# Kernel tuning notes

Measured on AMD Instinct MI355X. Metric: run time of the kernel, lower is better.

Reference implementation:

```python
import jax, jax.numpy as jnp
import numpy as np

SEQ, B, IN, H, OUT = 600, 4096, 6, 30, 61


def setup_inputs() -> dict:
    key = jax.random.key(0)
    ks = jax.random.split(key, 9)
    s_ih = 1.0 / np.sqrt(H)
    return {
        "X": jax.random.normal(ks[0], (SEQ, B, IN), dtype=jnp.float32),
        "W_ih": jax.random.uniform(ks[1], (4 * H, IN), jnp.float32, -s_ih, s_ih),
        "W_hh": jax.random.uniform(ks[2], (4 * H, H), jnp.float32, -s_ih, s_ih),
        "b_ih": jax.random.uniform(ks[3], (4 * H,), jnp.float32, -s_ih, s_ih),
        "b_hh": jax.random.uniform(ks[4], (4 * H,), jnp.float32, -s_ih, s_ih),
        "W1": jax.random.uniform(ks[5], (H, H), jnp.float32, -s_ih, s_ih),
        "b1": jax.random.uniform(ks[6], (H,), jnp.float32, -s_ih, s_ih),
        "W2": jax.random.uniform(ks[7], (OUT, H), jnp.float32, -s_ih, s_ih),
        "b2": jax.random.uniform(ks[8], (OUT,), jnp.float32, -s_ih, s_ih),
        "batch_size": B,
    }


def _lstm_last_h(X, W_ih, W_hh, b_ih, b_hh):
    # Precompute input projections for all timesteps: [T, B, 4H]
    xg = jnp.einsum("tbi,gi->tbg", X, W_ih) + b_ih + b_hh
    h0 = jnp.zeros((X.shape[1], W_hh.shape[1]), X.dtype)
    c0 = jnp.zeros_like(h0)

    def step(carry, xg_t):
        h, c = carry
        g = xg_t + h @ W_hh.T  # [B, 4H]
        i, f, gg, o = jnp.split(g, 4, axis=-1)  # PyTorch gate order i,f,g,o
        c = jax.nn.sigmoid(f) * c + jax.nn.sigmoid(i) * jnp.tanh(gg)
        h = jax.nn.sigmoid(o) * jnp.tanh(c)
        return (h, c), None

    (h, _), _ = jax.lax.scan(step, (h0, c0), xg)
    return h  # out[-1, :, :]


def reference(X, W_ih, W_hh, b_ih, b_hh, W1, b1, W2, b2, batch_size):
    h = _lstm_last_h(X, W_ih, W_hh, b_ih, b_hh)
    out = h @ W1.T + b1  # fc1
    # dropout(p=0.6) is identity in eval mode
    out = out @ W2.T + b2  # fc2
    return out  # [B, 61]
```

## Files before the change

kernel.cpp:

```cpp
#include <hip/hip_runtime.h>


#define SEQ   600
#define BATCH 4096
#define INP   6
#define HID   30
#define NOUT  61

typedef float f32x2 __attribute__((ext_vector_type(2)));

__device__ __forceinline__ float rcp_(float x)  { return __builtin_amdgcn_rcpf(x); }
__device__ __forceinline__ float exp2_(float x) { return __builtin_amdgcn_exp2f(x); }
#define LOG2E  1.4426950408889634f
#define LOG2E2 2.8853900817779268f

extern "C" __global__ void __launch_bounds__(64, 2)
lstm_fused4(const float* __restrict__ X,   const float* __restrict__ Wih,
            const float* __restrict__ Whh, const float* __restrict__ bih,
            const float* __restrict__ bhh, const float* __restrict__ W1,
            const float* __restrict__ b1,  const float* __restrict__ W2,
            const float* __restrict__ b2,  float* __restrict__ out)
{
    __shared__ float h_sh[2][32];
    __shared__ float o1_sh[2][32];

    const int lane = threadIdx.x;
    const int half = lane >> 5;
    const int u    = lane & 31;
    const int uu   = (u < HID) ? u : (HID - 1);
    const int b    = blockIdx.x * 2 + half;
    const bool act = (u < HID);

    h_sh[half][u] = 0.0f;

    const float* r0 = Whh + (0 * HID + uu) * HID;
    const float* r1 = Whh + (1 * HID + uu) * HID;
    const float* r2 = Whh + (2 * HID + uu) * HID;
    const float* r3 = Whh + (3 * HID + uu) * HID;

    f32x2 w0[15], w1[15], w2[15], w3[15];
    #pragma unroll
    for (int j = 0; j < 15; ++j) {
        asm volatile("global_load_dwordx2 %0, %1, off" : "=v"(w0[j]) : "v"(r0 + 2 * j));
        asm volatile("global_load_dwordx2 %0, %1, off" : "=v"(w1[j]) : "v"(r1 + 2 * j));
        asm volatile("global_load_dwordx2 %0, %1, off" : "=v"(w2[j]) : "v"(r2 + 2 * j));
        asm volatile("global_load_dwordx2 %0, %1, off" : "=v"(w3[j]) : "v"(r3 + 2 * j));
    }
    const float* s0 = Wih + (0 * HID + uu) * INP;
    const float* s1 = Wih + (1 * HID + uu) * INP;
    const float* s2 = Wih + (2 * HID + uu) * INP;
    const float* s3 = Wih + (3 * HID + uu) * INP;

    f32x2 xw0[3], xw1[3], xw2[3], xw3[3];
    #pragma unroll
    for (int j = 0; j < 3; ++j) {
        asm volatile("global_load_dwordx2 %0, %1, off" : "=v"(xw0[j]) : "v"(s0 + 2 * j));
        asm volatile("global_load_dwordx2 %0, %1, off" : "=v"(xw1[j]) : "v"(s1 + 2 * j));
        asm volatile("global_load_dwordx2 %0, %1, off" : "=v"(xw2[j]) : "v"(s2 + 2 * j));
        asm volatile("global_load_dwordx2 %0, %1, off" : "=v"(xw3[j]) : "v"(s3 + 2 * j));
    }
    asm volatile("s_waitcnt vmcnt(0)" ::: "memory");

    float bb0 = 0.f, bb1 = 0.f, bb2 = 0.f, bb3 = 0.f;
    if (act) {
        bb0 = bih[0 * HID + u] + bhh[0 * HID + u];
        bb1 = bih[1 * HID + u] + bhh[1 * HID + u];
        bb2 = bih[2 * HID + u] + bhh[2 * HID + u];
        bb3 = bih[3 * HID + u] + bhh[3 * HID + u];
    }
    asm volatile("" : "+v"(bb0), "+v"(bb1), "+v"(bb2), "+v"(bb3));

    float c = 0.f, h = 0.f;

    f32x2 xc0, xc1, xc2, xn0, xn1, xn2;
    {
        const f32x2* p = (const f32x2*)(X + (size_t)b * INP);
        xc0 = p[0]; xc1 = p[1]; xc2 = p[2];
    }
    asm volatile("s_waitcnt lgkmcnt(0)" ::: "memory");

    const float4* h4p = (const float4*)(&h_sh[half][0]);
    const f32x2*  h2p = (const f32x2*)(&h_sh[half][0]);

    for (int t = 0; t < SEQ; ++t) {
        const int tn = (t + 1 < SEQ) ? (t + 1) : (SEQ - 1);
        const f32x2* p = (const f32x2*)(X + ((size_t)tn * BATCH + b) * INP);
        xn0 = p[0]; xn1 = p[1]; xn2 = p[2];

        float4 H0 = h4p[0], H1 = h4p[1], H2 = h4p[2], H3 = h4p[3];
        float4 H4 = h4p[4], H5 = h4p[5], H6 = h4p[6];
        f32x2  Ht = h2p[14];

        f32x2 a0e = f32x2{bb0, 0.f}, a0o = (f32x2)0.f;
        f32x2 a1e = f32x2{bb1, 0.f}, a1o = (f32x2)0.f;
        f32x2 a2e = f32x2{bb2, 0.f}, a2o = (f32x2)0.f;
        f32x2 a3e = f32x2{bb3, 0.f}, a3o = (f32x2)0.f;

        #define PK4(J, HX, HY, E)  do {                                   \
            f32x2 hv = f32x2{HX, HY};                                     \
            a0##E = __builtin_elementwise_fma(w0[J], hv, a0##E);          \
            a1##E = __builtin_elementwise_fma(w1[J], hv, a1##E);          \
            a2##E = __builtin_elementwise_fma(w2[J], hv, a2##E);          \
            a3##E = __builtin_elementwise_fma(w3[J], hv, a3##E);          \
        } while (0)
        PK4(0,  H0.x, H0.y, e); PK4(1,  H0.z, H0.w, o);
        PK4(2,  H1.x, H1.y, e); PK4(3,  H1.z, H1.w, o);
        PK4(4,  H2.x, H2.y, e); PK4(5,  H2.z, H2.w, o);
        PK4(6,  H3.x, H3.y, e); PK4(7,  H3.z, H3.w, o);
        PK4(8,  H4.x, H4.y, e); PK4(9,  H4.z, H4.w, o);
        PK4(10, H5.x, H5.y, e); PK4(11, H5.z, H5.w, o);
        PK4(12, H6.x, H6.y, e); PK4(13, H6.z, H6.w, o);
        {
            a0e = __builtin_elementwise_fma(w0[14], Ht, a0e);
            a1e = __builtin_elementwise_fma(w1[14], Ht, a1e);
            a2e = __builtin_elementwise_fma(w2[14], Ht, a2e);
            a3e = __builtin_elementwise_fma(w3[14], Ht, a3e);
        }
        #undef PK4
        a0o = __builtin_elementwise_fma(xw0[0], xc0, a0o);
        a1o = __builtin_elementwise_fma(xw1[0], xc0, a1o);
        a2o = __builtin_elementwise_fma(xw2[0], xc0, a2o);
        a3o = __builtin_elementwise_fma(xw3[0], xc0, a3o);
        a0e = __builtin_elementwise_fma(xw0[1], xc1, a0e);
        a1e = __builtin_elementwise_fma(xw1[1], xc1, a1e);
        a2e = __builtin_elementwise_fma(xw2[1], xc1, a2e);
        a3e = __builtin_elementwise_fma(xw3[1], xc1, a3e);
        a0o = __builtin_elementwise_fma(xw0[2], xc2, a0o);
        a1o = __builtin_elementwise_fma(xw1[2], xc2, a1o);
        a2o = __builtin_elementwise_fma(xw2[2], xc2, a2o);
        a3o = __builtin_elementwise_fma(xw3[2], xc2, a3o);

        const f32x2 g0v = a0e + a0o, g1v = a1e + a1o;
        const f32x2 g2v = a2e + a2o, g3v = a3e + a3o;
        const float g0 = g0v.x + g0v.y;
        const float g1 = g1v.x + g1v.y;
        const float g2 = g2v.x + g2v.y;
        const float g3 = g3v.x + g3v.y;

        const float si = rcp_(1.0f + exp2_(-LOG2E * g0));
        const float sf = rcp_(1.0f + exp2_(-LOG2E * g1));
        const float tg = 1.0f - 2.0f * rcp_(exp2_(LOG2E2 * g2) + 1.0f);
        const float so = rcp_(1.0f + exp2_(-LOG2E * g3));

        c = fmaf(sf, c, si * tg);
        const float tc = 1.0f - 2.0f * rcp_(exp2_(LOG2E2 * c) + 1.0f);
        h = so * tc;

        if (act) h_sh[half][u] = h;
        asm volatile("s_waitcnt lgkmcnt(0)" ::: "memory");

        xc0 = xn0; xc1 = xn1; xc2 = xn2;
    }

    if (act) {
        float a1 = b1[u];
        const float* w1r = W1 + u * HID;
        #pragma unroll
        for (int k = 0; k < HID; ++k) a1 = fmaf(w1r[k], h_sh[half][k], a1);
        o1_sh[half][u] = a1;
    }
    asm volatile("s_waitcnt lgkmcnt(0)" ::: "memory");

    if (act) {
        for (int o = u; o < NOUT; o += HID) {
            float a2 = b2[o];
            const float* w2r = W2 + o * HID;
            #pragma unroll
            for (int k = 0; k < HID; ++k) a2 = fmaf(w2r[k], o1_sh[half][k], a2);
            out[(size_t)b * NOUT + o] = a2;
        }
    }
}

extern "C" void kernel_launch(void* const* d_in, const int* in_sizes, int n_in,
                              void* d_out, int out_size, void* d_ws, size_t ws_size,
                              hipStream_t stream) {
    const float* X   = (const float*)d_in[0];
    const float* Wih = (const float*)d_in[1];
    const float* Whh = (const float*)d_in[2];
    const float* bih = (const float*)d_in[3];
    const float* bhh = (const float*)d_in[4];
    const float* W1  = (const float*)d_in[5];
    const float* b1  = (const float*)d_in[6];
    const float* W2  = (const float*)d_in[7];
    const float* b2  = (const float*)d_in[8];
    float* out = (float*)d_out;

    dim3 grid(BATCH / 2);
    dim3 block(64);
    hipLaunchKernelGGL(lstm_fused4, grid, block, 0, stream,
                       X, Wih, Whh, bih, bhh, W1, b1, W2, b2, out);
}
```

Before: 350.2 us.

## Use packed fp16 dot2 for LSTM gate matvec with fp16 hidden state

Converts recurrent and input weights to packed fp16 once in registers and computes gate pre-activations with v_dot2 fp16 instructions that accumulate in fp32. The hidden state is stored in shared memory as fp16, so each step reads it with four 16-byte loads instead of seven float4 loads plus one f32x2 load. The input prefetch is restructured as a pointer walk with a peeled last step. This roughly halves the weight register footprint and the FMA count per step. The cost is reduced precision in the 600-step recurrence, and the saturating pkrtz conversion may accumulate error beyond tolerance.

After: 324.5 us. 1.08x faster.

```diff
diff --git a/kernel.cpp b/kernel.cpp
--- a/kernel.cpp
+++ b/kernel.cpp
@@ -7,21 +7,26 @@
 #define HID   30
 #define NOUT  61
 
+typedef __fp16 f16;
+typedef f16  f16x2 __attribute__((ext_vector_type(2)));
 typedef float f32x2 __attribute__((ext_vector_type(2)));
 
 __device__ __forceinline__ float rcp_(float x)  { return __builtin_amdgcn_rcpf(x); }
 __device__ __forceinline__ float exp2_(float x) { return __builtin_amdgcn_exp2f(x); }
+__device__ __forceinline__ f16x2 as_h2(unsigned v) {
+    union { unsigned u; f16x2 h; } c; c.u = v; return c.h;
+}
 #define LOG2E  1.4426950408889634f
 #define LOG2E2 2.8853900817779268f
 
 extern "C" __global__ void __launch_bounds__(64, 2)
-lstm_fused4(const float* __restrict__ X,   const float* __restrict__ Wih,
+lstm_fused9(const float* __restrict__ X,   const float* __restrict__ Wih,
             const float* __restrict__ Whh, const float* __restrict__ bih,
             const float* __restrict__ bhh, const float* __restrict__ W1,
             const float* __restrict__ b1,  const float* __restrict__ W2,
             const float* __restrict__ b2,  float* __restrict__ out)
 {
-    __shared__ float h_sh[2][32];
+    __shared__ __align__(16) f16 h_sh[2][32];
     __shared__ float o1_sh[2][32];
 
     const int lane = threadIdx.x;
@@ -31,35 +36,45 @@
     const int b    = blockIdx.x * 2 + half;
     const bool act = (u < HID);
 
-    h_sh[half][u] = 0.0f;
-
-    const float* r0 = Whh + (0 * HID + uu) * HID;
-    const float* r1 = Whh + (1 * HID + uu) * HID;
-    const float* r2 = Whh + (2 * HID + uu) * HID;
-    const float* r3 = Whh + (3 * HID + uu) * HID;
-
-    f32x2 w0[15], w1[15], w2[15], w3[15];
+    h_sh[half][u] = (f16)0.f;
+
+    f16x2 w0[15], w1[15], w2[15], w3[15];
+    f16x2 x0w[3], x1w[3], x2w[3], x3w[3];
+
+    #define LOADGATE(Q, WH, XW) do {                                          \
+        const float* rr = Whh + (Q * HID + uu) * HID;                         \
+        const float* ss = Wih + (Q * HID + uu) * INP;                         \
+        f32x2 t[15], tx[3];                                                   \
+        _Pragma("unroll")                                                     \
+        for (int j = 0; j < 15; ++j)                                          \
+            asm volatile("global_load_dwordx2 %0, %1, off"                    \
+                         : "=v"(t[j]) : "v"(rr + 2 * j));                     \
+        _Pragma("unroll")                                                     \
+        for (int j = 0; j < 3; ++j)                                           \
+            asm volatile("global_load_dwordx2 %0, %1, off"                    \
+                         : "=v"(tx[j]) : "v"(ss + 2 * j));                    \
+        asm volatile("s_waitcnt vmcnt(0)" ::: "memory");                      \
+        __builtin_amdgcn_sched_barrier(0);      \
+        _Pragma("unroll")                                                     \
+        for (int j = 0; j < 15; ++j)                                          \
+            WH[j] = __builtin_amdgcn_cvt_pkrtz(t[j].x, t[j].y);               \
+        _Pragma("unroll")                                                     \
+        for (int j = 0; j < 3; ++j)                                           \
+            XW[j] = __builtin_amdgcn_cvt_pkrtz(tx[j].x, tx[j].y);             \
+    } while (0)
+
+    LOADGATE(0, w0, x0w);
+    LOADGATE(1, w1, x1w);
+    LOADGATE(2, w2, x2w);
+    LOADGATE(3, w3, x3w);
+    #undef LOADGATE
+
     #pragma unroll
-    for (int j = 0; j < 15; ++j) {
-        asm volatile("global_load_dwordx2 %0, %1, off" : "=v"(w0[j]) : "v"(r0 + 2 * j));
-        asm volatile("global_load_dwordx2 %0, %1, off" : "=v"(w1[j]) : "v"(r1 + 2 * j));
-        asm volatile("global_load_dwordx2 %0, %1, off" : "=v"(w2[j]) : "v"(r2 + 2 * j));
-        asm volatile("global_load_dwordx2 %0, %1, off" : "=v"(w3[j]) : "v"(r3 + 2 * j));
-    }
-    const float* s0 = Wih + (0 * HID + uu) * INP;
-    const float* s1 = Wih + (1 * HID + uu) * INP;
-    const float* s2 = Wih + (2 * HID + uu) * INP;
-    const float* s3 = Wih + (3 * HID + uu) * INP;
-
-    f32x2 xw0[3], xw1[3], xw2[3], xw3[3];
+    for (int j = 0; j < 15; ++j)
+        asm("" : "+v"(w0[j]), "+v"(w1[j]), "+v"(w2[j]), "+v"(w3[j]));
     #pragma unroll
-    for (int j = 0; j < 3; ++j) {
-        asm volatile("global_load_dwordx2 %0, %1, off" : "=v"(xw0[j]) : "v"(s0 + 2 * j));
-        asm volatile("global_load_dwordx2 %0, %1, off" : "=v"(xw1[j]) : "v"(s1 + 2 * j));
-        asm volatile("global_load_dwordx2 %0, %1, off" : "=v"(xw2[j]) : "v"(s2 + 2 * j));
-        asm volatile("global_load_dwordx2 %0, %1, off" : "=v"(xw3[j]) : "v"(s3 + 2 * j));
-    }
-    asm volatile("s_waitcnt vmcnt(0)" ::: "memory");
+    for (int j = 0; j < 3; ++j)
+        asm("" : "+v"(x0w[j]), "+v"(x1w[j]), "+v"(x2w[j]), "+v"(x3w[j]));
 
     float bb0 = 0.f, bb1 = 0.f, bb2 = 0.f, bb3 = 0.f;
     if (act) {
@@ -68,95 +83,92 @@
         bb2 = bih[2 * HID + u] + bhh[2 * HID + u];
         bb3 = bih[3 * HID + u] + bhh[3 * HID + u];
     }
-    asm volatile("" : "+v"(bb0), "+v"(bb1), "+v"(bb2), "+v"(bb3));
-
-    float c = 0.f, h = 0.f;
-
-    f32x2 xc0, xc1, xc2, xn0, xn1, xn2;
+    asm("" : "+v"(bb0), "+v"(bb1), "+v"(bb2), "+v"(bb3));
+
+    float c = 0.f;
+
+    float4 xq; f32x2 xr;
     {
-        const f32x2* p = (const f32x2*)(X + (size_t)b * INP);
-        xc0 = p[0]; xc1 = p[1]; xc2 = p[2];
-    }
+        const float* p = X + (size_t)b * INP;
+        xq = *(const float4*)p;
+        xr = *(const f32x2*)(p + 4);
+    }
+    const float* pn = X + (size_t)BATCH * INP + (size_t)b * INP;
+
     asm volatile("s_waitcnt lgkmcnt(0)" ::: "memory");
 
-    const float4* h4p = (const float4*)(&h_sh[half][0]);
-    const f32x2*  h2p = (const f32x2*)(&h_sh[half][0]);
-
-    for (int t = 0; t < SEQ; ++t) {
-        const int tn = (t + 1 < SEQ) ? (t + 1) : (SEQ - 1);
-        const f32x2* p = (const f32x2*)(X + ((size_t)tn * BATCH + b) * INP);
-        xn0 = p[0]; xn1 = p[1]; xn2 = p[2];
-
-        float4 H0 = h4p[0], H1 = h4p[1], H2 = h4p[2], H3 = h4p[3];
-        float4 H4 = h4p[4], H5 = h4p[5], H6 = h4p[6];
-        f32x2  Ht = h2p[14];
-
-        f32x2 a0e = f32x2{bb0, 0.f}, a0o = (f32x2)0.f;
-        f32x2 a1e = f32x2{bb1, 0.f}, a1o = (f32x2)0.f;
-        f32x2 a2e = f32x2{bb2, 0.f}, a2o = (f32x2)0.f;
-        f32x2 a3e = f32x2{bb3, 0.f}, a3o = (f32x2)0.f;
-
-        #define PK4(J, HX, HY, E)  do {                                   \
-            f32x2 hv = f32x2{HX, HY};                                     \
-            a0##E = __builtin_elementwise_fma(w0[J], hv, a0##E);          \
-            a1##E = __builtin_elementwise_fma(w1[J], hv, a1##E);          \
-            a2##E = __builtin_elementwise_fma(w2[J], hv, a2##E);          \
-            a3##E = __builtin_elementwise_fma(w3[J], hv, a3##E);          \
-        } while (0)
-        PK4(0,  H0.x, H0.y, e); PK4(1,  H0.z, H0.w, o);
-        PK4(2,  H1.x, H1.y, e); PK4(3,  H1.z, H1.w, o);
-        PK4(4,  H2.x, H2.y, e); PK4(5,  H2.z, H2.w, o);
-        PK4(6,  H3.x, H3.y, e); PK4(7,  H3.z, H3.w, o);
-        PK4(8,  H4.x, H4.y, e); PK4(9,  H4.z, H4.w, o);
-        PK4(10, H5.x, H5.y, e); PK4(11, H5.z, H5.w, o);
-        PK4(12, H6.x, H6.y, e); PK4(13, H6.z, H6.w, o);
-        {
-            a0e = __builtin_elementwise_fma(w0[14], Ht, a0e);
-            a1e = __builtin_elementwise_fma(w1[14], Ht, a1e);
-            a2e = __builtin_elementwise_fma(w2[14], Ht, a2e);
-            a3e = __builtin_elementwise_fma(w3[14], Ht, a3e);
-        }
-        #undef PK4
-        a0o = __builtin_elementwise_fma(xw0[0], xc0, a0o);
-        a1o = __builtin_elementwise_fma(xw1[0], xc0, a1o);
-        a2o = __builtin_elementwise_fma(xw2[0], xc0, a2o);
-        a3o = __builtin_elementwise_fma(xw3[0], xc0, a3o);
-        a0e = __builtin_elementwise_fma(xw0[1], xc1, a0e);
-        a1e = __builtin_elementwise_fma(xw1[1], xc1, a1e);
-        a2e = __builtin_elementwise_fma(xw2[1], xc1, a2e);
-        a3e = __builtin_elementwise_fma(xw3[1], xc1, a3e);
-        a0o = __builtin_elementwise_fma(xw0[2], xc2, a0o);
-        a1o = __builtin_elementwise_fma(xw1[2], xc2, a1o);
-        a2o = __builtin_elementwise_fma(xw2[2], xc2, a2o);
-        a3o = __builtin_elementwise_fma(xw3[2], xc2, a3o);
-
-        const f32x2 g0v = a0e + a0o, g1v = a1e + a1o;
-        const f32x2 g2v = a2e + a2o, g3v = a3e + a3o;
-        const float g0 = g0v.x + g0v.y;
-        const float g1 = g1v.x + g1v.y;
-        const float g2 = g2v.x + g2v.y;
-        const float g3 = g3v.x + g3v.y;
-
-        const float si = rcp_(1.0f + exp2_(-LOG2E * g0));
-        const float sf = rcp_(1.0f + exp2_(-LOG2E * g1));
-        const float tg = 1.0f - 2.0f * rcp_(exp2_(LOG2E2 * g2) + 1.0f);
-        const float so = rcp_(1.0f + exp2_(-LOG2E * g3));
-
-        c = fmaf(sf, c, si * tg);
-        const float tc = 1.0f - 2.0f * rcp_(exp2_(LOG2E2 * c) + 1.0f);
-        h = so * tc;
-
-        if (act) h_sh[half][u] = h;
-        asm volatile("s_waitcnt lgkmcnt(0)" ::: "memory");
-
-        xc0 = xn0; xc1 = xn1; xc2 = xn2;
-    }
+    const uint4* hq = (const uint4*)(&h_sh[half][0]);
+
+    #define DO_STEP() do {                                                    \
+        const f16x2 xh0 = __builtin_amdgcn_cvt_pkrtz(xq.x, xq.y);             \
+        const f16x2 xh1 = __builtin_amdgcn_cvt_pkrtz(xq.z, xq.w);             \
+        const f16x2 xh2 = __builtin_amdgcn_cvt_pkrtz(xr.x, xr.y);             \
+        const uint4 Q0 = hq[0], Q1 = hq[1], Q2 = hq[2], Q3 = hq[3];           \
+        const f16x2 hp[16] = {                                                \
+            as_h2(Q0.x), as_h2(Q0.y), as_h2(Q0.z), as_h2(Q0.w),               \
+            as_h2(Q1.x), as_h2(Q1.y), as_h2(Q1.z), as_h2(Q1.w),               \
+            as_h2(Q2.x), as_h2(Q2.y), as_h2(Q2.z), as_h2(Q2.w),               \
+            as_h2(Q3.x), as_h2(Q3.y), as_h2(Q3.z), as_h2(Q3.w)               \
+        };                                                                    \
+        float a0e = bb0, a0o = 0.f, a1e = bb1, a1o = 0.f;                     \
+        float a2e = bb2, a2o = 0.f, a3e = bb3, a3o = 0.f;                     \
+        _Pragma("unroll")                                                     \
+        for (int j = 0; j < 15; j += 2) {                                     \
+            a0e = __builtin_amdgcn_fdot2(w0[j], hp[j], a0e, false);           \
+            a1e = __builtin_amdgcn_fdot2(w1[j], hp[j], a1e, false);           \
+            a2e = __builtin_amdgcn_fdot2(w2[j], hp[j], a2e, false);           \
+            a3e = __builtin_amdgcn_fdot2(w3[j], hp[j], a3e, false);           \
+            if (j + 1 < 15) {                                                 \
+                a0o = __builtin_amdgcn_fdot2(w0[j+1], hp[j+1], a0o, false);   \
+                a1o = __builtin_amdgcn_fdot2(w1[j+1], hp[j+1], a1o, false);   \
+                a2o = __builtin_amdgcn_fdot2(w2[j+1], hp[j+1], a2o, false);   \
+                a3o = __builtin_amdgcn_fdot2(w3[j+1], hp[j+1], a3o, false);   \
+            }                                                                 \
+        }                                                                     \
+        a0o = __builtin_amdgcn_fdot2(x0w[0], xh0, a0o, false);                \
+        a1o = __builtin_amdgcn_fdot2(x1w[0], xh0, a1o, false);                \
+        a2o = __builtin_amdgcn_fdot2(x2w[0], xh0, a2o, false);                \
+        a3o = __builtin_amdgcn_fdot2(x3w[0], xh0, a3o, false);                \
+        a0e = __builtin_amdgcn_fdot2(x0w[1], xh1, a0e, false);                \
+        a1e = __builtin_amdgcn_fdot2(x1w[1], xh1, a1e, false);                \
+        a2e = __builtin_amdgcn_fdot2(x2w[1], xh1, a2e, false);                \
+        a3e = __builtin_amdgcn_fdot2(x3w[1], xh1, a3e, false);                \
+        a0o = __builtin_amdgcn_fdot2(x0w[2], xh2, a0o, false);                \
+        a1o = __builtin_amdgcn_fdot2(x1w[2], xh2, a1o, false);                \
+        a2o = __builtin_amdgcn_fdot2(x2w[2], xh2, a2o, false);                \
+        a3o = __builtin_amdgcn_fdot2(x3w[2], xh2, a3o, false);                \
+        const float g0 = a0e + a0o;                                    \
+        const float g1 = a1e + a1o;                                    \
+        const float g2 = a2e + a2o;                                    \
+        const float g3 = a3e + a3o;                                    \
+        const float si = rcp_(1.0f + exp2_(-LOG2E * g0));                     \
+        const float sf = rcp_(1.0f + exp2_(-LOG2E * g1));                     \
+        const float tg = 1.0f - 2.0f * rcp_(exp2_(LOG2E2 * g2) + 1.0f);       \
+        const float so = rcp_(1.0f + exp2_(-LOG2E * g3));                     \
+        c = fmaf(sf, c, si * tg);                                             \
+        const float tc = 1.0f - 2.0f * rcp_(exp2_(LOG2E2 * c) + 1.0f);        \
+        const float hv = so * tc;                                             \
+        if (act) h_sh[half][u] = (f16)hv;                                     \
+        asm volatile("s_waitcnt lgkmcnt(0)" ::: "memory");                    \
+    } while (0)
+
+    for (int t = 0; t < SEQ - 1; ++t) {
+        const float4 yq = *(const float4*)pn;
+        const f32x2 yr = *(const f32x2*)(pn + 4);
+        pn += (size_t)BATCH * INP;
+
+        DO_STEP();
+
+        xq = yq; xr = yr;
+    }
+    DO_STEP();
+    #undef DO_STEP
 
     if (act) {
         float a1 = b1[u];
         const float* w1r = W1 + u * HID;
         #pragma unroll
-        for (int k = 0; k < HID; ++k) a1 = fmaf(w1r[k], h_sh[half][k], a1);
+        for (int k = 0; k < HID; ++k) a1 = fmaf(w1r[k], (float)h_sh[half][k], a1);
         o1_sh[half][u] = a1;
     }
     asm volatile("s_waitcnt lgkmcnt(0)" ::: "memory");
@@ -188,6 +200,6 @@
 
     dim3 grid(BATCH / 2);
     dim3 block(64);
-    hipLaunchKernelGGL(lstm_fused4, grid, block, 0, stream,
+    hipLaunchKernelGGL(lstm_fused9, grid, block, 0, stream,
                        X, Wih, Whh, bih, bhh, W1, b1, W2, b2, out);
 }
```
